# Performance work log

Measured on AMD Instinct MI355X. Metric: run time of the kernel, lower is better.

The kernel has to match this reference:

```python
import jax, jax.numpy as jnp
import numpy as np
from jax import lax

D_MODEL = 1024
D_INNER = 2048   # expand * d_model
D_STATE = 16
D_CONV = 4
DT_RANK = 64     # ceil(d_model / 16)
B_SZ, L_SEQ = 2, 2048


def setup_inputs() -> dict:
    key = jax.random.key(0)
    ks = jax.random.split(key, 12)
    s = lambda *sh: 1.0 / np.sqrt(sh[-1])
    inp = {
        "x": jax.random.normal(ks[0], (B_SZ, L_SEQ, D_MODEL), jnp.float32),
        "in_proj_w": jax.random.normal(ks[1], (2 * D_INNER, D_MODEL), jnp.float32) * s(D_MODEL),
        "conv_w": jax.random.normal(ks[2], (D_INNER, 1, D_CONV), jnp.float32) * 0.3,
        "conv_b": jax.random.normal(ks[3], (D_INNER,), jnp.float32) * 0.05,
        "x_proj_w": jax.random.normal(ks[4], (DT_RANK + 2 * D_STATE, D_INNER), jnp.float32) * s(D_INNER),
        "dt_proj_w": jax.random.normal(ks[5], (D_INNER, DT_RANK), jnp.float32) * s(DT_RANK),
        "dt_proj_b": jnp.log(jnp.exp(jax.random.uniform(ks[6], (D_INNER,), jnp.float32, 1e-3, 1e-1)) - 1.0),
        "A_log": jnp.log(jnp.broadcast_to(jnp.arange(1, D_STATE + 1, dtype=jnp.float32), (D_INNER, D_STATE))),
        "D": jnp.ones((D_INNER,), jnp.float32),
        "out_proj_w": jax.random.normal(ks[7], (D_MODEL, D_INNER), jnp.float32) * s(D_INNER),
        "ln_w": jnp.ones((D_MODEL,), jnp.float32),
        "ln_b": jnp.zeros((D_MODEL,), jnp.float32),
    }
    return inp


def _mamba(x, in_proj_w, conv_w, conv_b, x_proj_w, dt_proj_w, dt_proj_b, A_log, D, out_proj_w):
    # x: [B, L, d_model]
    xz = x @ in_proj_w.T                             # [B, L, 2*d_inner]
    u, z = jnp.split(xz, 2, axis=-1)                 # [B, L, d_inner] each
    # depthwise causal conv1d along L
    u_c = jnp.swapaxes(u, 1, 2)                      # [B, d_inner, L]
    u_c = lax.conv_general_dilated(
        u_c, conv_w, window_strides=(1,), padding=[(D_CONV - 1, 0)],
        feature_group_count=D_INNER, dimension_numbers=("NCH", "OIH", "NCH"))
    u_c = u_c + conv_b[None, :, None]
    u_c = jax.nn.silu(jnp.swapaxes(u_c, 1, 2))       # [B, L, d_inner]
    # input-dependent dt, B, C
    x_dbl = u_c @ x_proj_w.T                         # [B, L, dt_rank + 2*d_state]
    dt_lr = x_dbl[..., :DT_RANK]
    Bm = x_dbl[..., DT_RANK:DT_RANK + D_STATE]       # [B, L, d_state]
    Cm = x_dbl[..., DT_RANK + D_STATE:]              # [B, L, d_state]
    dt = jax.nn.softplus(dt_lr @ dt_proj_w.T + dt_proj_b)  # [B, L, d_inner]
    A = -jnp.exp(A_log)                              # [d_inner, d_state]

    def step(h, inputs):
        dt_t, b_t, c_t, u_t = inputs                 # [B,d_inner],[B,N],[B,N],[B,d_inner]
        dA = jnp.exp(dt_t[:, :, None] * A)           # [B, d_inner, N]
        h = h * dA + (dt_t * u_t)[:, :, None] * b_t[:, None, :]
        y_t = jnp.einsum("bdn,bn->bd", h, c_t)
        return h, y_t

    h0 = jnp.zeros((x.shape[0], D_INNER, D_STATE), x.dtype)
    xs = (jnp.swapaxes(dt, 0, 1), jnp.swapaxes(Bm, 0, 1),
          jnp.swapaxes(Cm, 0, 1), jnp.swapaxes(u_c, 0, 1))
    _, ys = lax.scan(step, h0, xs)                   # ys: [L, B, d_inner]
    y = jnp.swapaxes(ys, 0, 1) + u_c * D             # skip connection D*u
    y = y * jax.nn.silu(z)                           # gate
    return y @ out_proj_w.T                          # [B, L, d_model]


def _layernorm(x, w, b, eps=1e-5):
    mu = jnp.mean(x, axis=-1, keepdims=True)
    var = jnp.mean(jnp.square(x - mu), axis=-1, keepdims=True)
    return (x - mu) * lax.rsqrt(var + eps) * w + b


def reference(x, in_proj_w, conv_w, conv_b, x_proj_w, dt_proj_w, dt_proj_b,
              A_log, D, out_proj_w, ln_w, ln_b):
    y = _mamba(x, in_proj_w, conv_w, conv_b, x_proj_w, dt_proj_w, dt_proj_b,
               A_log, D, out_proj_w)
    return _layernorm(y + x, ln_w, ln_b)  # dropout_level=0 -> identity
```

## Files before the change

kernel.cpp:

```cpp
#include <hip/hip_runtime.h>
#include <hip/hip_bf16.h>
#include <math.h>

#define DEV static __device__ __forceinline__

typedef __hip_bfloat16 bf16;
typedef __attribute__((ext_vector_type(8))) short bf16x8;
typedef __attribute__((ext_vector_type(4))) short bf16x4;
typedef __attribute__((ext_vector_type(4))) float f32x4;

static constexpr int D_MODEL = 1024;
static constexpr int D_INNER = 2048;
static constexpr int D_STATE = 16;
static constexpr int DT_RANK = 64;
static constexpr int B_SZ   = 2;
static constexpr int L_SEQ  = 2048;
static constexpr int T_TOK  = B_SZ * L_SEQ;
static constexpr int LC     = 64;
static constexpr int NC     = L_SEQ / LC;
static constexpr int NXP    = DT_RANK + 2 * D_STATE;
static constexpr int KSPLIT = 8;

static constexpr int P_CONVW = 0;
static constexpr int P_CONVB = 8192;
static constexpr int P_DTB   = 10240;
static constexpr int P_ALOG  = 12288;
static constexpr int P_DW    = 45056;
static constexpr int P_LNW   = 47104;
static constexpr int P_LNB   = 48128;
static constexpr int P_TOT   = 49152;

DEV float bf2f(bf16 x) { return __bfloat162float(x); }
DEV bf16  f2bf(float x) { return __float2bfloat16(x); }
DEV float sigmoidf_(float x) { return 1.0f / (1.0f + __expf(-x)); }
DEV float s2f(short s) { bf16 b; __builtin_memcpy(&b, &s, 2); return bf2f(b); }
DEV short f2s(float x) { bf16 b = f2bf(x); short s; __builtin_memcpy(&s, &b, 2); return s; }

DEV bool probe_f32(const unsigned short* probe) { return probe[1] == 0; }

DEV void async_copy16(const void* g, void* l) {
  __builtin_amdgcn_global_load_lds(
      (const __attribute__((address_space(1))) void*)g,
      (__attribute__((address_space(3))) void*)l, 16, 0, 0);
}

__global__ void cvt_all(const void* s0, const void* s1, const void* s2,
                        const void* s3, const void* s4,
                        const void* s5, const void* s6, const void* s7,
                        const void* s8, const void* s9, const void* s10,
                        const void* s11,
                        bf16* d0, bf16* d1, bf16* d2, bf16* d3, bf16* d4,
                        float* params,
                        const unsigned short* __restrict__ probe)
{
  long i = (long)(blockIdx.x * 256 + threadIdx.x) * 4;
  const void* src; long off;
  bf16* dstb = nullptr; float* dstf = nullptr;
  if      (i <  4194304) { src = s0;  dstb = d0; off = i; }
  else if (i <  8388608) { src = s1;  dstb = d1; off = i - 4194304; }
  else if (i <  8585216) { src = s2;  dstb = d2; off = i - 8388608; }
  else if (i <  8716288) { src = s3;  dstb = d3; off = i - 8585216; }
  else if (i < 10813440) { src = s4;  dstb = d4; off = i - 8716288; }
  else if (i < 10821632) { src = s5;  dstf = params + P_CONVW; off = i - 10813440; }
  else if (i < 10823680) { src = s6;  dstf = params + P_CONVB; off = i - 10821632; }
  else if (i < 10825728) { src = s7;  dstf = params + P_DTB;   off = i - 10823680; }
  else if (i < 10858496) { src = s8;  dstf = params + P_ALOG;  off = i - 10825728; }
  else if (i < 10860544) { src = s9;  dstf = params + P_DW;    off = i - 10858496; }
  else if (i < 10861568) { src = s10; dstf = params + P_LNW;   off = i - 10860544; }
  else if (i < 10862592) { src = s11; dstf = params + P_LNB;   off = i - 10861568; }
  else return;
  bool isf32 = probe_f32(probe);
  float v[4];
  if (isf32) {
    float4 t = *(const float4*)((const float*)src + off);
    v[0] = t.x; v[1] = t.y; v[2] = t.z; v[3] = t.w;
  } else {
    short4 t = *(const short4*)((const bf16*)src + off);
    v[0] = s2f(t.x); v[1] = s2f(t.y); v[2] = s2f(t.z); v[3] = s2f(t.w);
  }
  if (dstb) {
    #pragma unroll
    for (int k = 0; k < 4; ++k) dstb[off + k] = f2bf(v[k]);
  } else {
    #pragma unroll
    for (int k = 0; k < 4; ++k) dstf[off + k] = v[k];
  }
}

template <int MODE>
DEV void gemm_body64(const bf16* __restrict__ A, const bf16* __restrict__ B,
                     int M, int N, int K, int ld,
                     void* __restrict__ o0, void* __restrict__ o1)
{
  __shared__ __align__(16) bf16 As[128 * 64];
  __shared__ __align__(16) bf16 Bs[128 * 64];
  if (MODE == 3) {
    A += (size_t)blockIdx.z * K;
    B += (size_t)blockIdx.z * K;
  }
  const int tid  = threadIdx.x;
  const int wave = tid >> 6;
  const int lane = tid & 63;
  const int bm = blockIdx.x * 128;
  const int bn = blockIdx.y * 128;
  const int wm = (wave >> 1) * 64;
  const int wn = (wave & 1) * 64;

  f32x4 acc[4][4];
  #pragma unroll
  for (int i = 0; i < 4; ++i)
    #pragma unroll
    for (int j = 0; j < 4; ++j)
      #pragma unroll
      for (int r = 0; r < 4; ++r) acc[i][j][r] = 0.0f;

  const int srow8 = lane >> 3;
  const int sgcol = ((lane & 7) ^ srow8) * 8;
  const int fr = lane & 15;
  const int fq = lane >> 4;

  for (int k0 = 0; k0 < K; k0 += 64) {
    __syncthreads();
    #pragma unroll
    for (int rep = 0; rep < 4; ++rep) {
      int chunk = wave * 4 + rep;
      int arow = bm + chunk * 8 + srow8;
      async_copy16((const void*)(A + (size_t)arow * ld + k0 + sgcol),
                   (void*)(As + chunk * 512));
      int brow = bn + chunk * 8 + srow8;
      if (brow > N - 1) brow = N - 1;
      async_copy16((const void*)(B + (size_t)brow * ld + k0 + sgcol),
                   (void*)(Bs + chunk * 512));
    }
    __syncthreads();

    #pragma unroll
    for (int kk = 0; kk < 2; ++kk) {
      bf16x8 af[4], bg[4];
      #pragma unroll
      for (int mi = 0; mi < 4; ++mi) {
        int row = wm + mi * 16 + fr;
        af[mi] = *(const bf16x8*)(As + row * 64 + (((kk * 4 + fq) ^ (fr & 7)) * 8));
      }
      #pragma unroll
      for (int ni = 0; ni < 4; ++ni) {
        int row = wn + ni * 16 + fr;
        bg[ni] = *(const bf16x8*)(Bs + row * 64 + (((kk * 4 + fq) ^ (fr & 7)) * 8));
      }
      #pragma unroll
      for (int mi = 0; mi < 4; ++mi)
        #pragma unroll
        for (int ni = 0; ni < 4; ++ni)
          acc[mi][ni] = __builtin_amdgcn_mfma_f32_16x16x32_bf16(af[mi], bg[ni], acc[mi][ni], 0, 0, 0);
    }
  }

  const int er = (lane >> 4) * 4;
  const int ec = lane & 15;
  #pragma unroll
  for (int mi = 0; mi < 4; ++mi) {
    #pragma unroll
    for (int ni = 0; ni < 4; ++ni) {
      #pragma unroll
      for (int r = 0; r < 4; ++r) {
        int row = bm + wm + mi * 16 + er + r;
        int col = bn + wn + ni * 16 + ec;
        float v = acc[mi][ni][r];
        if (MODE == 0) {
          if (col < D_INNER) ((bf16*)o0)[(size_t)row * D_INNER + col] = f2bf(v);
          else               ((bf16*)o1)[(size_t)row * D_INNER + (col - D_INNER)] = f2bf(v * sigmoidf_(v));
        } else {
          ((bf16*)o0)[((size_t)blockIdx.z * M + row) * D_MODEL + col] = f2bf(v);
        }
      }
    }
  }
}

template <int MODE>
DEV void gemm_body32(const bf16* __restrict__ A, const bf16* __restrict__ B,
                     int M, int N, int K, int ld,
                     void* __restrict__ o0, const void* __restrict__ e0)
{
  __shared__ __align__(16) bf16 As[128 * 32];
  __shared__ __align__(16) bf16 Bs[128 * 32];
  if (MODE == 1) {
    A += (size_t)blockIdx.z * K;
    B += (size_t)blockIdx.z * K;
  }
  const int tid  = threadIdx.x;
  const int wave = tid >> 6;
  const int lane = tid & 63;
  const int bm = blockIdx.x * 128;
  const int bn = blockIdx.y * 128;
  const int wm = (wave >> 1) * 64;
  const int wn = (wave & 1) * 64;

  f32x4 acc[4][4];
  #pragma unroll
  for (int i = 0; i < 4; ++i)
    #pragma unroll
    for (int j = 0; j < 4; ++j)
      #pragma unroll
      for (int r = 0; r < 4; ++r) acc[i][j][r] = 0.0f;

  const int ar0 = tid >> 2;
  const int ar1 = ar0 + 64;
  const int ac  = (tid & 3) * 8;
  const int fr = lane & 15;
  const int fk = (lane >> 4) * 8;

  for (int k0 = 0; k0 < K; k0 += 32) {
    bf16x8 a0 = *(const bf16x8*)(A + (size_t)(bm + ar0) * ld + k0 + ac);
    bf16x8 a1 = *(const bf16x8*)(A + (size_t)(bm + ar1) * ld + k0 + ac);
    int r0 = bn + ar0; if (r0 > N - 1) r0 = N - 1;
    int r1 = bn + ar1; if (r1 > N - 1) r1 = N - 1;
    bf16x8 b0 = *(const bf16x8*)(B + (size_t)r0 * ld + k0 + ac);
    bf16x8 b1 = *(const bf16x8*)(B + (size_t)r1 * ld + k0 + ac);
    __syncthreads();
    *(bf16x8*)(As + ar0 * 32 + ac) = a0;
    *(bf16x8*)(As + ar1 * 32 + ac) = a1;
    *(bf16x8*)(Bs + ar0 * 32 + ac) = b0;
    *(bf16x8*)(Bs + ar1 * 32 + ac) = b1;
    __syncthreads();

    bf16x8 af[4], bg[4];
    #pragma unroll
    for (int mi = 0; mi < 4; ++mi)
      af[mi] = *(const bf16x8*)(As + (wm + mi * 16 + fr) * 32 + fk);
    #pragma unroll
    for (int ni = 0; ni < 4; ++ni)
      bg[ni] = *(const bf16x8*)(Bs + (wn + ni * 16 + fr) * 32 + fk);
    #pragma unroll
    for (int mi = 0; mi < 4; ++mi)
      #pragma unroll
      for (int ni = 0; ni < 4; ++ni)
        acc[mi][ni] = __builtin_amdgcn_mfma_f32_16x16x32_bf16(af[mi], bg[ni], acc[mi][ni], 0, 0, 0);
  }

  const int er = (lane >> 4) * 4;
  const int ec = lane & 15;
  #pragma unroll
  for (int mi = 0; mi < 4; ++mi) {
    #pragma unroll
    for (int ni = 0; ni < 4; ++ni) {
      #pragma unroll
      for (int r = 0; r < 4; ++r) {
        int row = bm + wm + mi * 16 + er + r;
        int col = bn + wn + ni * 16 + ec;
        if (col >= N) continue;
        float v = acc[mi][ni][r];
        if (MODE == 1) {
          ((float*)o0)[((size_t)blockIdx.z * M + row) * N + col] = v;
        } else {
          v += ((const float*)e0)[col];
          float sp = (v > 15.0f) ? v : __logf(1.0f + __expf(v));
          ((bf16*)o0)[(size_t)row * D_INNER + col] = f2bf(sp);
        }
      }
    }
  }
}

__global__ void __launch_bounds__(256) k_inproj(const bf16* A, const bf16* B,
    void* o0, void* o1) {
  gemm_body64<0>(A, B, T_TOK, 2 * D_INNER, D_MODEL, D_MODEL, o0, o1);
}
__global__ void __launch_bounds__(256) k_outproj(const bf16* A, const bf16* B,
    void* o0) {
  gemm_body64<3>(A, B, T_TOK, D_MODEL, D_INNER / 2, D_INNER, o0, nullptr);
}
__global__ void __launch_bounds__(256) k_xproj(const bf16* A, const bf16* B,
    void* o0) {
  gemm_body32<1>(A, B, T_TOK, NXP, D_INNER / KSPLIT, D_INNER, o0, nullptr);
}
__global__ void __launch_bounds__(256) k_dtproj(const bf16* A, const bf16* B,
    void* o0, const void* e0) {
  gemm_body32<2>(A, B, T_TOK, D_INNER, DT_RANK, DT_RANK, o0, e0);
}

__global__ void xproj_post(const float* __restrict__ partials,
                           bf16* __restrict__ dtlr,
                           float* __restrict__ Bbuf,
                           float* __restrict__ Cbuf)
{
  int i = blockIdx.x * 256 + threadIdx.x;
  int col = i % NXP;
  int row = i / NXP;
  float s = 0.0f;
  #pragma unroll
  for (int kz = 0; kz < KSPLIT; ++kz)
    s += partials[((size_t)kz * T_TOK + row) * NXP + col];
  if      (col < DT_RANK)            dtlr[(size_t)row * DT_RANK + col] = f2bf(s);
  else if (col < DT_RANK + D_STATE)  Bbuf[(size_t)row * D_STATE + (col - DT_RANK)] = s;
  else                               Cbuf[(size_t)row * D_STATE + (col - DT_RANK - D_STATE)] = s;
}

__global__ void conv_silu_kernel(const bf16* __restrict__ u_pre,
                                 const float* __restrict__ cw,
                                 const float* __restrict__ cb,
                                 bf16* __restrict__ uc_bf)
{
  int idx = blockIdx.x * 256 + threadIdx.x;
  int d4 = (idx * 4) & (D_INNER - 1);
  int t  = (idx * 4) >> 11;
  int l  = t & (L_SEQ - 1);
  float4 bias = *(const float4*)(cb + d4);
  float acc[4] = {bias.x, bias.y, bias.z, bias.w};
  float4 wv[4];
  #pragma unroll
  for (int i = 0; i < 4; ++i) wv[i] = *(const float4*)(cw + (d4 + i) * 4);
  #pragma unroll
  for (int w = 0; w < 4; ++w) {
    if (l - 3 + w >= 0) {
      bf16x4 u = *(const bf16x4*)(u_pre + (size_t)(t - 3 + w) * D_INNER + d4);
      float uf[4];
      #pragma unroll
      for (int i = 0; i < 4; ++i) { short su = u[i]; uf[i] = s2f(su); }
      acc[0] += uf[0] * ((const float*)&wv[0])[w];
      acc[1] += uf[1] * ((const float*)&wv[1])[w];
      acc[2] += uf[2] * ((const float*)&wv[2])[w];
      acc[3] += uf[3] * ((const float*)&wv[3])[w];
    }
  }
  bf16x4 out;
  #pragma unroll
  for (int i = 0; i < 4; ++i) out[i] = f2s(acc[i] * sigmoidf_(acc[i]));
  *(bf16x4*)(uc_bf + (size_t)t * D_INNER + d4) = out;
}

DEV void load_Ad(const float* A_log, int d, float* Ad, bool& fast) {
  fast = true;
  #pragma unroll
  for (int n = 0; n < 16; ++n) {
    Ad[n] = -__expf(A_log[d * 16 + n]);
    fast = fast && (fabsf(Ad[n] + (float)(n + 1)) < 1e-3f * (n + 1));
  }
}
DEV void compute_decay(bool fast, float dtv, const float* Ad, float* dec) {
  if (fast) {
    float e1 = __expf(-dtv);
    float en = e1;
    #pragma unroll
    for (int n = 0; n < 16; ++n) { dec[n] = en; en *= e1; }
  } else {
    #pragma unroll
    for (int n = 0; n < 16; ++n) dec[n] = __expf(Ad[n] * dtv);
  }
}

__global__ __launch_bounds__(256) void scan_pass1(
    const bf16* __restrict__ dt, const bf16* __restrict__ uc_bf,
    const float* __restrict__ Bbuf, const float* __restrict__ A_log,
    float* __restrict__ hend, float* __restrict__ sumdt)
{
  __shared__ float Bs4[LC * D_STATE];
  __shared__ bf16 dts[16 * 256];
  __shared__ bf16 uts[16 * 256];
  int bid = blockIdx.x;
  int tid = threadIdx.x;
  int dt8 = bid & 7;
  int c = (bid >> 3) & (NC - 1);
  int b = bid >> 8;
  int d0 = dt8 * 256;
  int d  = d0 + tid;
  int t0g = b * L_SEQ + c * LC;

  ((f32x4*)Bs4)[tid] = ((const f32x4*)(Bbuf + (size_t)t0g * D_STATE))[tid];

  float Ad[16], h[16];
  bool fast;
  load_Ad(A_log, d, Ad, fast);
  #pragma unroll
  for (int n = 0; n < 16; ++n) h[n] = 0.0f;
  float sdt = 0.0f;

  for (int sub = 0; sub < 4; ++sub) {
    __syncthreads();
    #pragma unroll
    for (int rep = 0; rep < 2; ++rep) {
      int idx = rep * 256 + tid;
      int row = idx >> 5;
      int col = (idx & 31) * 8;
      size_t src = (size_t)(t0g + sub * 16 + row) * D_INNER + d0 + col;
      *(bf16x8*)(dts + row * 256 + col) = *(const bf16x8*)(dt + src);
      *(bf16x8*)(uts + row * 256 + col) = *(const bf16x8*)(uc_bf + src);
    }
    __syncthreads();
    for (int t = 0; t < 16; ++t) {
      float dtv = bf2f(dts[t * 256 + tid]);
      float uv  = bf2f(uts[t * 256 + tid]);
      float su  = dtv * uv;
      sdt += dtv;
      float dec[16];
      compute_decay(fast, dtv, Ad, dec);
      const float* Bp = Bs4 + (sub * 16 + t) * 16;
      #pragma unroll
      for (int n = 0; n < 16; ++n)
        h[n] = h[n] * dec[n] + su * Bp[n];
    }
  }
  size_t base = ((size_t)(b * NC + c) * D_INNER + d) * 16;
  #pragma unroll
  for (int q = 0; q < 4; ++q)
    *(f32x4*)(hend + base + q * 4) = *(f32x4*)(h + q * 4);
  sumdt[(size_t)(b * NC + c) * D_INNER + d] = sdt;
}

__global__ __launch_bounds__(256) void scan_pass2(
    float* __restrict__ hend, const float* __restrict__ sumdt,
    const float* __restrict__ A_log)
{
  __shared__ float Ms[4][64];
  __shared__ float Es[4][64];
  int bid = blockIdx.x;
  int tid = threadIdx.x;
  int cg   = tid >> 6;
  int lane = tid & 63;
  int dloc = lane >> 4;
  int n    = lane & 15;
  int b     = bid >> 9;
  int d     = (bid & 511) * 4 + dloc;

  float a = -__expf(A_log[d * 16 + n]);

  float Ml[8], El[8];
  float M = 1.0f, E = 0.0f;
  #pragma unroll
  for (int j = 0; j < 8; ++j) {
    int c = cg * 8 + j;
    size_t sbase = (size_t)(b * NC + c) * D_INNER + d;
    float m = __expf(a * sumdt[sbase]);
    float e = hend[sbase * 16 + n];
    Ml[j] = M; El[j] = E;
    M = m * M;
    E = m * E + e;
  }
  Ms[cg][lane] = M;
  Es[cg][lane] = E;
  __syncthreads();
  float Ep = 0.0f;
  for (int g = 0; g < cg; ++g) {
    float Mg = Ms[g][lane], Eg = Es[g][lane];
    Ep = Mg * Ep + Eg;
  }
  #pragma unroll
  for (int j = 0; j < 8; ++j) {
    int c = cg * 8 + j;
    size_t sbase = (size_t)(b * NC + c) * D_INNER + d;
    hend[sbase * 16 + n] = Ml[j] * Ep + El[j];
  }
}

__global__ __launch_bounds__(256) void scan_pass3(
    const bf16* __restrict__ dt, const bf16* __restrict__ uc_bf,
    const float* __restrict__ Bbuf, const float* __restrict__ Cbuf,
    const bf16* __restrict__ z_silu, const float* __restrict__ hstart,
    const float* __restrict__ A_log, const float* __restrict__ Dw,
    bf16* __restrict__ y_bf)
{
  __shared__ float Bs4[LC * D_STATE];
  __shared__ float Cs4[LC * D_STATE];
  __shared__ bf16 dts[16 * 256];
  __shared__ bf16 uts[16 * 256];
  __shared__ bf16 zts[16 * 256];
  int bid = blockIdx.x;
  int tid = threadIdx.x;
  int dt8 = bid & 7;
  int c = (bid >> 3) & (NC - 1);
  int b = bid >> 8;
  int d0 = dt8 * 256;
  int d  = d0 + tid;
  int t0g = b * L_SEQ + c * LC;

  ((f32x4*)Bs4)[tid] = ((const f32x4*)(Bbuf + (size_t)t0g * D_STATE))[tid];
  ((f32x4*)Cs4)[tid] = ((const f32x4*)(Cbuf + (size_t)t0g * D_STATE))[tid];

  float Ad[16], h[16];
  bool fast;
  load_Ad(A_log, d, Ad, fast);
  size_t base = ((size_t)(b * NC + c) * D_INNER + d) * 16;
  #pragma unroll
  for (int q = 0; q < 4; ++q)
    *(f32x4*)(h + q * 4) = *(const f32x4*)(hstart + base + q * 4);
  float Dv = Dw[d];

  for (int sub = 0; sub < 4; ++sub) {
    __syncthreads();
    #pragma unroll
    for (int rep = 0; rep < 2; ++rep) {
      int idx = rep * 256 + tid;
      int row = idx >> 5;
      int col = (idx & 31) * 8;
      size_t src = (size_t)(t0g + sub * 16 + row) * D_INNER + d0 + col;
      *(bf16x8*)(dts + row * 256 + col) = *(const bf16x8*)(dt + src);
      *(bf16x8*)(uts + row * 256 + col) = *(const bf16x8*)(uc_bf + src);
      *(bf16x8*)(zts + row * 256 + col) = *(const bf16x8*)(z_silu + src);
    }
    __syncthreads();
    for (int t = 0; t < 16; ++t) {
      float dtv = bf2f(dts[t * 256 + tid]);
      float uv  = bf2f(uts[t * 256 + tid]);
      float zv  = bf2f(zts[t * 256 + tid]);
      float su  = dtv * uv;
      float dec[16];
      compute_decay(fast, dtv, Ad, dec);
      const float* Bp = Bs4 + (sub * 16 + t) * 16;
      const float* Cp = Cs4 + (sub * 16 + t) * 16;
      float y = 0.0f;
      #pragma unroll
      for (int n = 0; n < 16; ++n) {
        h[n] = h[n] * dec[n] + su * Bp[n];
        y += h[n] * Cp[n];
      }
      y = (y + uv * Dv) * zv;
      y_bf[(size_t)(t0g + sub * 16 + t) * D_INNER + d] = f2bf(y);
    }
  }
}

__global__ void ln_kernel(const bf16* __restrict__ parts,
                          const bf16* __restrict__ x_bf,
                          const float* __restrict__ w,
                          const float* __restrict__ bia,
                          void* __restrict__ out,
                          const unsigned short* __restrict__ probe)
{
  int t = blockIdx.x;
  int tid = threadIdx.x;
  const bf16* p0 = parts + (size_t)t * D_MODEL;
  const bf16* p1 = parts + ((size_t)T_TOK + t) * D_MODEL;
  const bf16* xr = x_bf + (size_t)t * D_MODEL;
  float v[4];
  float s = 0.0f, q = 0.0f;
  #pragma unroll
  for (int k = 0; k < 4; ++k) {
    int col = tid + k * 256;
    v[k] = bf2f(p0[col]) + bf2f(p1[col]) + bf2f(xr[col]);
    s += v[k]; q += v[k] * v[k];
  }
  #pragma unroll
  for (int off = 32; off >= 1; off >>= 1) {
    s += __shfl_down(s, off);
    q += __shfl_down(q, off);
  }
  __shared__ float red[8];
  __shared__ float mv[2];
  int wave = tid >> 6, lane = tid & 63;
  if (lane == 0) { red[wave] = s; red[4 + wave] = q; }
  __syncthreads();
  if (tid == 0) {
    float S = red[0] + red[1] + red[2] + red[3];
    float Q = red[4] + red[5] + red[6] + red[7];
    float mu = S * (1.0f / D_MODEL);
    float var = Q * (1.0f / D_MODEL) - mu * mu;
    mv[0] = mu; mv[1] = rsqrtf(var + 1e-5f);
  }
  __syncthreads();
  float mu = mv[0], rs = mv[1];
  bool isf32 = probe_f32(probe);
  #pragma unroll
  for (int k = 0; k < 4; ++k) {
    int col = tid + k * 256;
    float r = (v[k] - mu) * rs * w[col] + bia[col];
    if (isf32) ((float*)out)[(size_t)t * D_MODEL + col] = r;
    else       ((bf16*) out)[(size_t)t * D_MODEL + col] = f2bf(r);
  }
}

extern "C" void kernel_launch(void* const* d_in, const int* in_sizes, int n_in,
                              void* d_out, int out_size, void* d_ws, size_t ws_size,
                              hipStream_t stream)
{
  const void* x        = d_in[0];
  const void* in_w     = d_in[1];
  const void* conv_w   = d_in[2];
  const void* conv_b   = d_in[3];
  const void* xproj_w  = d_in[4];
  const void* dtproj_w = d_in[5];
  const void* dtproj_b = d_in[6];
  const void* A_log    = d_in[7];
  const void* Dw       = d_in[8];
  const void* out_w    = d_in[9];
  const void* ln_w     = d_in[10];
  const void* ln_b     = d_in[11];
  const unsigned short* probe = (const unsigned short*)A_log;

  char* p = (char*)d_ws;
  auto alloc = [&](size_t bytes) { char* r = p; p += (bytes + 255) & ~255ull; return r; };
  bf16*  x_bf   = (bf16*) alloc((size_t)T_TOK * D_MODEL * 2);
  bf16*  inw_bf = (bf16*) alloc((size_t)2 * D_INNER * D_MODEL * 2);
  bf16*  xpw_bf = (bf16*) alloc((size_t)NXP * D_INNER * 2);
  bf16*  dtw_bf = (bf16*) alloc((size_t)D_INNER * DT_RANK * 2);
  bf16*  outw_bf= (bf16*) alloc((size_t)D_MODEL * D_INNER * 2);
  float* params = (float*)alloc((size_t)P_TOT * 4);
  bf16*  u_pre  = (bf16*) alloc((size_t)T_TOK * D_INNER * 2);
  bf16*  z_silu = (bf16*) alloc((size_t)T_TOK * D_INNER * 2);
  bf16*  uc_bf  = (bf16*) alloc((size_t)T_TOK * D_INNER * 2);
  bf16*  dtlr   = (bf16*) alloc((size_t)T_TOK * DT_RANK * 2);
  float* Bbuf   = (float*)alloc((size_t)T_TOK * D_STATE * 4);
  float* Cbuf   = (float*)alloc((size_t)T_TOK * D_STATE * 4);
  bf16*  dtb    = (bf16*) alloc((size_t)T_TOK * D_INNER * 2);
  float* hend   = (float*)alloc((size_t)B_SZ * NC * D_INNER * 16 * 4);
  float* sumdt  = (float*)alloc((size_t)B_SZ * NC * D_INNER * 4);
  bf16*  y_bf   = u_pre;
  float* xparts = (float*)dtb;
  bf16*  oparts = z_silu;

  dim3 blk(256);
  cvt_all<<<10608, blk, 0, stream>>>(x, in_w, xproj_w, dtproj_w, out_w,
                                     conv_w, conv_b, dtproj_b, A_log, Dw, ln_w, ln_b,
                                     x_bf, inw_bf, xpw_bf, dtw_bf, outw_bf, params, probe);

  k_inproj<<<dim3(T_TOK / 128, (2 * D_INNER) / 128), blk, 0, stream>>>(x_bf, inw_bf, u_pre, z_silu);
  conv_silu_kernel<<<(T_TOK * D_INNER) / 1024, blk, 0, stream>>>(u_pre, params + P_CONVW, params + P_CONVB, uc_bf);
  k_xproj<<<dim3(T_TOK / 128, 1, KSPLIT), blk, 0, stream>>>(uc_bf, xpw_bf, xparts);
  xproj_post<<<(T_TOK * NXP) / 256, blk, 0, stream>>>(xparts, dtlr, Bbuf, Cbuf);
  k_dtproj<<<dim3(T_TOK / 128, D_INNER / 128), blk, 0, stream>>>(dtlr, dtw_bf, dtb, params + P_DTB);
  scan_pass1<<<B_SZ * NC * (D_INNER / 256), blk, 0, stream>>>(dtb, uc_bf, Bbuf, params + P_ALOG, hend, sumdt);
  scan_pass2<<<(B_SZ * D_INNER) / 2, blk, 0, stream>>>(hend, sumdt, params + P_ALOG);
  scan_pass3<<<B_SZ * NC * (D_INNER / 256), blk, 0, stream>>>(
      dtb, uc_bf, Bbuf, Cbuf, z_silu, hend, params + P_ALOG, params + P_DW, y_bf);
  k_outproj<<<dim3(T_TOK / 128, D_MODEL / 128, 2), blk, 0, stream>>>(y_bf, outw_bf, oparts);
  ln_kernel<<<T_TOK, blk, 0, stream>>>(oparts, x_bf, params + P_LNW, params + P_LNB, d_out, probe);
}
```

Baseline: 307.1 us.

## Pipeline in/out projection GEMMs with 4-slot async LDS ring and 8 waves

```diff
diff --git a/kernel.cpp b/kernel.cpp
--- a/kernel.cpp
+++ b/kernel.cpp
@@ -42,6 +42,13 @@
   __builtin_amdgcn_global_load_lds(
       (const __attribute__((address_space(1))) void*)g,
       (__attribute__((address_space(3))) void*)l, 16, 0, 0);
+}
+
+template <int N>
+DEV void vm_wait() {
+  if constexpr (N == 6)      asm volatile("s_waitcnt vmcnt(6)" ::: "memory");
+  else if constexpr (N == 3) asm volatile("s_waitcnt vmcnt(3)" ::: "memory");
+  else                       asm volatile("s_waitcnt vmcnt(0)" ::: "memory");
 }
 
 __global__ void cvt_all(const void* s0, const void* s1, const void* s2,
@@ -87,13 +94,37 @@
   }
 }
 
+static constexpr int SLOT_BYTES = 256 * 32 * 2 + 128 * 32 * 2;
+static constexpr int B_OFF      = 256 * 32 * 2;
+
+DEV void stage_slot(const bf16* __restrict__ A, const bf16* __restrict__ B,
+                    int ld, int bm, int bn, int k0,
+                    char* slot, int wave, int lane)
+{
+  const int tid = wave * 64 + lane;
+  #pragma unroll
+  for (int j = 0; j < 2; ++j) {
+    int p   = j * 8192 + tid * 16;
+    int row = p >> 6;
+    int ckl = ((p >> 4) & 3) ^ (row & 3);
+    async_copy16(A + (size_t)(bm + row) * ld + k0 + ckl * 8,
+                 slot + j * 8192 + wave * 1024);
+  }
+  {
+    int p   = tid * 16;
+    int row = p >> 6;
+    int ckl = ((p >> 4) & 3) ^ (row & 3);
+    async_copy16(B + (size_t)(bn + row) * ld + k0 + ckl * 8,
+                 slot + B_OFF + wave * 1024);
+  }
+}
+
 template <int MODE>
-DEV void gemm_body64(const bf16* __restrict__ A, const bf16* __restrict__ B,
+DEV void gemm8p_body(const bf16* __restrict__ A, const bf16* __restrict__ B,
                      int M, int N, int K, int ld,
                      void* __restrict__ o0, void* __restrict__ o1)
 {
-  __shared__ __align__(16) bf16 As[128 * 64];
-  __shared__ __align__(16) bf16 Bs[128 * 64];
+  __shared__ __align__(16) char ring[4 * SLOT_BYTES];
   if (MODE == 3) {
     A += (size_t)blockIdx.z * K;
     B += (size_t)blockIdx.z * K;
@@ -101,10 +132,16 @@
   const int tid  = threadIdx.x;
   const int wave = tid >> 6;
   const int lane = tid & 63;
-  const int bm = blockIdx.x * 128;
+  const int bm = blockIdx.x * 256;
   const int bn = blockIdx.y * 128;
-  const int wm = (wave >> 1) * 64;
-  const int wn = (wave & 1) * 64;
+  const int wm = wave >> 1;
+  const int wn = wave & 1;
+  const int fr = lane & 15;
+  const int fg = lane >> 4;
+  const int sck = ((fg ^ (fr & 3)) << 4);
+  const int abase = (wm * 64 + fr) * 64 + sck;
+  const int bbase = B_OFF + (wn * 64 + fr) * 64 + sck;
+  const int NT = K / 32;
 
   f32x4 acc[4][4];
   #pragma unroll
@@ -114,45 +151,41 @@
       #pragma unroll
       for (int r = 0; r < 4; ++r) acc[i][j][r] = 0.0f;
 
-  const int srow8 = lane >> 3;
-  const int sgcol = ((lane & 7) ^ srow8) * 8;
-  const int fr = lane & 15;
-  const int fq = lane >> 4;
-
-  for (int k0 = 0; k0 < K; k0 += 64) {
-    __syncthreads();
-    #pragma unroll
-    for (int rep = 0; rep < 4; ++rep) {
-      int chunk = wave * 4 + rep;
-      int arow = bm + chunk * 8 + srow8;
-      async_copy16((const void*)(A + (size_t)arow * ld + k0 + sgcol),
-                   (void*)(As + chunk * 512));
-      int brow = bn + chunk * 8 + srow8;
-      if (brow > N - 1) brow = N - 1;
-      async_copy16((const void*)(B + (size_t)brow * ld + k0 + sgcol),
-                   (void*)(Bs + chunk * 512));
-    }
-    __syncthreads();
-
-    #pragma unroll
-    for (int kk = 0; kk < 2; ++kk) {
-      bf16x8 af[4], bg[4];
-      #pragma unroll
-      for (int mi = 0; mi < 4; ++mi) {
-        int row = wm + mi * 16 + fr;
-        af[mi] = *(const bf16x8*)(As + row * 64 + (((kk * 4 + fq) ^ (fr & 7)) * 8));
-      }
-      #pragma unroll
-      for (int ni = 0; ni < 4; ++ni) {
-        int row = wn + ni * 16 + fr;
-        bg[ni] = *(const bf16x8*)(Bs + row * 64 + (((kk * 4 + fq) ^ (fr & 7)) * 8));
-      }
-      #pragma unroll
-      for (int mi = 0; mi < 4; ++mi)
-        #pragma unroll
-        for (int ni = 0; ni < 4; ++ni)
-          acc[mi][ni] = __builtin_amdgcn_mfma_f32_16x16x32_bf16(af[mi], bg[ni], acc[mi][ni], 0, 0, 0);
-    }
+  #pragma unroll
+  for (int u = 0; u < 3; ++u)
+    stage_slot(A, B, ld, bm, bn, u * 32, ring + u * SLOT_BYTES, wave, lane);
+
+  for (int t = 0; t < NT; ++t) {
+    if (t < NT - 2)       vm_wait<6>();
+    else if (t == NT - 2) vm_wait<3>();
+    else                  vm_wait<0>();
+    __builtin_amdgcn_sched_barrier(0);
+    __builtin_amdgcn_s_barrier();
+    __builtin_amdgcn_sched_barrier(0);
+
+    const char* sb = ring + (t & 3) * SLOT_BYTES;
+    bf16x8 af[4], bg[4];
+    #pragma unroll
+    for (int mi = 0; mi < 4; ++mi)
+      af[mi] = *(const bf16x8*)(sb + abase + mi * 1024);
+    #pragma unroll
+    for (int ni = 0; ni < 4; ++ni)
+      bg[ni] = *(const bf16x8*)(sb + bbase + ni * 1024);
+    __builtin_amdgcn_sched_barrier(0);
+
+    if (t + 3 < NT)
+      stage_slot(A, B, ld, bm, bn, (t + 3) * 32,
+                 ring + ((t + 3) & 3) * SLOT_BYTES, wave, lane);
+    __builtin_amdgcn_sched_barrier(0);
+
+    __builtin_amdgcn_s_setprio(1);
+    #pragma unroll
+    for (int mi = 0; mi < 4; ++mi)
+      #pragma unroll
+      for (int ni = 0; ni < 4; ++ni)
+        acc[mi][ni] = __builtin_amdgcn_mfma_f32_16x16x32_bf16(af[mi], bg[ni], acc[mi][ni], 0, 0, 0);
+    __builtin_amdgcn_s_setprio(0);
+    __builtin_amdgcn_sched_barrier(0);
   }
 
   const int er = (lane >> 4) * 4;
@@ -163,8 +196,8 @@
     for (int ni = 0; ni < 4; ++ni) {
       #pragma unroll
       for (int r = 0; r < 4; ++r) {
-        int row = bm + wm + mi * 16 + er + r;
-        int col = bn + wn + ni * 16 + ec;
+        int row = bm + wm * 64 + mi * 16 + er + r;
+        int col = bn + wn * 64 + ni * 16 + ec;
         float v = acc[mi][ni][r];
         if (MODE == 0) {
           if (col < D_INNER) ((bf16*)o0)[(size_t)row * D_INNER + col] = f2bf(v);
@@ -262,13 +295,13 @@
   }
 }
 
-__global__ void __launch_bounds__(256) k_inproj(const bf16* A, const bf16* B,
+__global__ void __launch_bounds__(512) k_inproj(const bf16* A, const bf16* B,
     void* o0, void* o1) {
-  gemm_body64<0>(A, B, T_TOK, 2 * D_INNER, D_MODEL, D_MODEL, o0, o1);
-}
-__global__ void __launch_bounds__(256) k_outproj(const bf16* A, const bf16* B,
+  gemm8p_body<0>(A, B, T_TOK, 2 * D_INNER, D_MODEL, D_MODEL, o0, o1);
+}
+__global__ void __launch_bounds__(512) k_outproj(const bf16* A, const bf16* B,
     void* o0) {
-  gemm_body64<3>(A, B, T_TOK, D_MODEL, D_INNER / 2, D_INNER, o0, nullptr);
+  gemm8p_body<3>(A, B, T_TOK, D_MODEL, D_INNER / 2, D_INNER, o0, nullptr);
 }
 __global__ void __launch_bounds__(256) k_xproj(const bf16* A, const bf16* B,
     void* o0) {
@@ -608,11 +641,12 @@
   bf16*  oparts = z_silu;
 
   dim3 blk(256);
+  dim3 blk512(512);
   cvt_all<<<10608, blk, 0, stream>>>(x, in_w, xproj_w, dtproj_w, out_w,
                                      conv_w, conv_b, dtproj_b, A_log, Dw, ln_w, ln_b,
                                      x_bf, inw_bf, xpw_bf, dtw_bf, outw_bf, params, probe);
 
-  k_inproj<<<dim3(T_TOK / 128, (2 * D_INNER) / 128), blk, 0, stream>>>(x_bf, inw_bf, u_pre, z_silu);
+  k_inproj<<<dim3(T_TOK / 256, (2 * D_INNER) / 128), blk512, 0, stream>>>(x_bf, inw_bf, u_pre, z_silu);
   conv_silu_kernel<<<(T_TOK * D_INNER) / 1024, blk, 0, stream>>>(u_pre, params + P_CONVW, params + P_CONVB, uc_bf);
   k_xproj<<<dim3(T_TOK / 128, 1, KSPLIT), blk, 0, stream>>>(uc_bf, xpw_bf, xparts);
   xproj_post<<<(T_TOK * NXP) / 256, blk, 0, stream>>>(xparts, dtlr, Bbuf, Cbuf);
@@ -621,6 +655,6 @@
   scan_pass2<<<(B_SZ * D_INNER) / 2, blk, 0, stream>>>(hend, sumdt, params + P_ALOG);
   scan_pass3<<<B_SZ * NC * (D_INNER / 256), blk, 0, stream>>>(
       dtb, uc_bf, Bbuf, Cbuf, z_silu, hend, params + P_ALOG, params + P_DW, y_bf);
-  k_outproj<<<dim3(T_TOK / 128, D_MODEL / 128, 2), blk, 0, stream>>>(y_bf, outw_bf, oparts);
+  k_outproj<<<dim3(T_TOK / 256, D_MODEL / 128, 2), blk512, 0, stream>>>(y_bf, outw_bf, oparts);
   ln_kernel<<<T_TOK, blk, 0, stream>>>(oparts, x_bf, params + P_LNW, params + P_LNB, d_out, probe);
 }
```

After: 311.3 us. No clear change (+1.4%).

## Pipeline in/out-proj GEMMs with triple-buffered LDS ring and 256x128 tiles

Applied to the files above, without the earlier changes.

```diff
diff --git a/kernel.cpp b/kernel.cpp
--- a/kernel.cpp
+++ b/kernel.cpp
@@ -42,6 +42,12 @@
   __builtin_amdgcn_global_load_lds(
       (const __attribute__((address_space(1))) void*)g,
       (__attribute__((address_space(3))) void*)l, 16, 0, 0);
+}
+
+template <int N>
+DEV void vm_wait() {
+  if constexpr (N == 6) asm volatile("s_waitcnt vmcnt(6)" ::: "memory");
+  else                  asm volatile("s_waitcnt vmcnt(0)" ::: "memory");
 }
 
 __global__ void cvt_all(const void* s0, const void* s1, const void* s2,
@@ -87,13 +93,39 @@
   }
 }
 
+static constexpr int SLOT = 48 * 1024;
+static constexpr int BOFF = 32 * 1024;
+
+DEV void stage_A(const bf16* __restrict__ A, int ld, int bm, int k0,
+                 char* slot, int tid) {
+  #pragma unroll
+  for (int j = 0; j < 4; ++j) {
+    int p   = j * 8192 + tid * 16;
+    int row = p >> 7;
+    int ck  = ((p >> 4) & 7) ^ (row & 7);
+    async_copy16(A + (size_t)(bm + row) * ld + k0 + ck * 8,
+                 slot + j * 8192 + (tid >> 6) * 1024);
+  }
+}
+
+DEV void stage_B(const bf16* __restrict__ B, int ld, int bn, int k0,
+                 char* slot, int tid) {
+  #pragma unroll
+  for (int j = 0; j < 2; ++j) {
+    int p   = j * 8192 + tid * 16;
+    int row = p >> 7;
+    int ck  = ((p >> 4) & 7) ^ (row & 7);
+    async_copy16(B + (size_t)(bn + row) * ld + k0 + ck * 8,
+                 slot + BOFF + j * 8192 + (tid >> 6) * 1024);
+  }
+}
+
 template <int MODE>
-DEV void gemm_body64(const bf16* __restrict__ A, const bf16* __restrict__ B,
-                     int M, int N, int K, int ld,
-                     void* __restrict__ o0, void* __restrict__ o1)
-{
-  __shared__ __align__(16) bf16 As[128 * 64];
-  __shared__ __align__(16) bf16 Bs[128 * 64];
+DEV void gemm_pipe(const bf16* __restrict__ A, const bf16* __restrict__ B,
+                   int M, int K, int ld,
+                   void* __restrict__ o0, void* __restrict__ o1)
+{
+  __shared__ __align__(16) char ring[3 * SLOT];
   if (MODE == 3) {
     A += (size_t)blockIdx.z * K;
     B += (size_t)blockIdx.z * K;
@@ -101,58 +133,96 @@
   const int tid  = threadIdx.x;
   const int wave = tid >> 6;
   const int lane = tid & 63;
-  const int bm = blockIdx.x * 128;
+  const int bm = blockIdx.x * 256;
   const int bn = blockIdx.y * 128;
   const int wm = (wave >> 1) * 64;
   const int wn = (wave & 1) * 64;
-
-  f32x4 acc[4][4];
-  #pragma unroll
-  for (int i = 0; i < 4; ++i)
-    #pragma unroll
-    for (int j = 0; j < 4; ++j)
-      #pragma unroll
-      for (int r = 0; r < 4; ++r) acc[i][j][r] = 0.0f;
-
-  const int srow8 = lane >> 3;
-  const int sgcol = ((lane & 7) ^ srow8) * 8;
   const int fr = lane & 15;
   const int fq = lane >> 4;
-
-  for (int k0 = 0; k0 < K; k0 += 64) {
-    __syncthreads();
-    #pragma unroll
-    for (int rep = 0; rep < 4; ++rep) {
-      int chunk = wave * 4 + rep;
-      int arow = bm + chunk * 8 + srow8;
-      async_copy16((const void*)(A + (size_t)arow * ld + k0 + sgcol),
-                   (void*)(As + chunk * 512));
-      int brow = bn + chunk * 8 + srow8;
-      if (brow > N - 1) brow = N - 1;
-      async_copy16((const void*)(B + (size_t)brow * ld + k0 + sgcol),
-                   (void*)(Bs + chunk * 512));
-    }
-    __syncthreads();
-
-    #pragma unroll
-    for (int kk = 0; kk < 2; ++kk) {
-      bf16x8 af[4], bg[4];
-      #pragma unroll
-      for (int mi = 0; mi < 4; ++mi) {
+  const int NT = K / 64;
+
+  f32x4 acc[4][4];
+  #pragma unroll
+  for (int i = 0; i < 4; ++i)
+    #pragma unroll
+    for (int j = 0; j < 4; ++j)
+      #pragma unroll
+      for (int r = 0; r < 4; ++r) acc[i][j][r] = 0.0f;
+
+  stage_A(A, ld, bm, 0,  ring,        tid);
+  stage_B(B, ld, bn, 0,  ring,        tid);
+  stage_A(A, ld, bm, 64, ring + SLOT, tid);
+  stage_B(B, ld, bn, 64, ring + SLOT, tid);
+
+  int scur = 0;
+  #pragma unroll 1
+  for (int tk = 0; tk < NT; ++tk) {
+    if (tk < NT - 1) vm_wait<6>();
+    else             vm_wait<0>();
+    __builtin_amdgcn_sched_barrier(0);
+    __builtin_amdgcn_s_barrier();
+    __builtin_amdgcn_sched_barrier(0);
+
+    const char* sa = ring + scur * SLOT;
+    int snxt = scur + 2; if (snxt >= 3) snxt -= 3;
+    char* sn = ring + snxt * SLOT;
+
+    bf16x8 af[4][2], bg[2][2];
+    #pragma unroll
+    for (int mi = 0; mi < 4; ++mi)
+      #pragma unroll
+      for (int kk = 0; kk < 2; ++kk) {
         int row = wm + mi * 16 + fr;
-        af[mi] = *(const bf16x8*)(As + row * 64 + (((kk * 4 + fq) ^ (fr & 7)) * 8));
+        af[mi][kk] = *(const bf16x8*)(sa + row * 128 + (((kk * 4 + fq) ^ (fr & 7)) * 16));
       }
-      #pragma unroll
-      for (int ni = 0; ni < 4; ++ni) {
+    #pragma unroll
+    for (int ni = 0; ni < 2; ++ni)
+      #pragma unroll
+      for (int kk = 0; kk < 2; ++kk) {
         int row = wn + ni * 16 + fr;
-        bg[ni] = *(const bf16x8*)(Bs + row * 64 + (((kk * 4 + fq) ^ (fr & 7)) * 8));
+        bg[ni][kk] = *(const bf16x8*)(sa + BOFF + row * 128 + (((kk * 4 + fq) ^ (fr & 7)) * 16));
       }
+    __builtin_amdgcn_sched_barrier(0);
+    if (tk + 2 < NT) stage_A(A, ld, bm, (tk + 2) * 64, sn, tid);
+    __builtin_amdgcn_sched_barrier(0);
+    asm volatile("s_waitcnt lgkmcnt(0)" ::: "memory");
+    __builtin_amdgcn_sched_barrier(0);
+    __builtin_amdgcn_s_setprio(1);
+    #pragma unroll
+    for (int kk = 0; kk < 2; ++kk)
       #pragma unroll
       for (int mi = 0; mi < 4; ++mi)
         #pragma unroll
-        for (int ni = 0; ni < 4; ++ni)
-          acc[mi][ni] = __builtin_amdgcn_mfma_f32_16x16x32_bf16(af[mi], bg[ni], acc[mi][ni], 0, 0, 0);
-    }
+        for (int ni = 0; ni < 2; ++ni)
+          acc[mi][ni] = __builtin_amdgcn_mfma_f32_16x16x32_bf16(af[mi][kk], bg[ni][kk], acc[mi][ni], 0, 0, 0);
+    __builtin_amdgcn_s_setprio(0);
+    __builtin_amdgcn_sched_barrier(0);
+
+    bf16x8 bh[2][2];
+    #pragma unroll
+    for (int ni = 0; ni < 2; ++ni)
+      #pragma unroll
+      for (int kk = 0; kk < 2; ++kk) {
+        int row = wn + (ni + 2) * 16 + fr;
+        bh[ni][kk] = *(const bf16x8*)(sa + BOFF + row * 128 + (((kk * 4 + fq) ^ (fr & 7)) * 16));
+      }
+    __builtin_amdgcn_sched_barrier(0);
+    if (tk + 2 < NT) stage_B(B, ld, bn, (tk + 2) * 64, sn, tid);
+    __builtin_amdgcn_sched_barrier(0);
+    asm volatile("s_waitcnt lgkmcnt(0)" ::: "memory");
+    __builtin_amdgcn_sched_barrier(0);
+    __builtin_amdgcn_s_setprio(1);
+    #pragma unroll
+    for (int kk = 0; kk < 2; ++kk)
+      #pragma unroll
+      for (int mi = 0; mi < 4; ++mi)
+        #pragma unroll
+        for (int ni = 0; ni < 2; ++ni)
+          acc[mi][ni + 2] = __builtin_amdgcn_mfma_f32_16x16x32_bf16(af[mi][kk], bh[ni][kk], acc[mi][ni + 2], 0, 0, 0);
+    __builtin_amdgcn_s_setprio(0);
+    __builtin_amdgcn_sched_barrier(0);
+
+    scur = (scur + 1 == 3) ? 0 : scur + 1;
   }
 
   const int er = (lane >> 4) * 4;
@@ -262,13 +332,13 @@
   }
 }
 
-__global__ void __launch_bounds__(256) k_inproj(const bf16* A, const bf16* B,
+__global__ void __launch_bounds__(512) k_inproj(const bf16* A, const bf16* B,
     void* o0, void* o1) {
-  gemm_body64<0>(A, B, T_TOK, 2 * D_INNER, D_MODEL, D_MODEL, o0, o1);
-}
-__global__ void __launch_bounds__(256) k_outproj(const bf16* A, const bf16* B,
+  gemm_pipe<0>(A, B, T_TOK, D_MODEL, D_MODEL, o0, o1);
+}
+__global__ void __launch_bounds__(512) k_outproj(const bf16* A, const bf16* B,
     void* o0) {
-  gemm_body64<3>(A, B, T_TOK, D_MODEL, D_INNER / 2, D_INNER, o0, nullptr);
+  gemm_pipe<3>(A, B, T_TOK, D_INNER / 2, D_INNER, o0, nullptr);
 }
 __global__ void __launch_bounds__(256) k_xproj(const bf16* A, const bf16* B,
     void* o0) {
@@ -608,11 +678,12 @@
   bf16*  oparts = z_silu;
 
   dim3 blk(256);
+  dim3 blk512(512);
   cvt_all<<<10608, blk, 0, stream>>>(x, in_w, xproj_w, dtproj_w, out_w,
                                      conv_w, conv_b, dtproj_b, A_log, Dw, ln_w, ln_b,
                                      x_bf, inw_bf, xpw_bf, dtw_bf, outw_bf, params, probe);
 
-  k_inproj<<<dim3(T_TOK / 128, (2 * D_INNER) / 128), blk, 0, stream>>>(x_bf, inw_bf, u_pre, z_silu);
+  k_inproj<<<dim3(T_TOK / 256, (2 * D_INNER) / 128), blk512, 0, stream>>>(x_bf, inw_bf, u_pre, z_silu);
   conv_silu_kernel<<<(T_TOK * D_INNER) / 1024, blk, 0, stream>>>(u_pre, params + P_CONVW, params + P_CONVB, uc_bf);
   k_xproj<<<dim3(T_TOK / 128, 1, KSPLIT), blk, 0, stream>>>(uc_bf, xpw_bf, xparts);
   xproj_post<<<(T_TOK * NXP) / 256, blk, 0, stream>>>(xparts, dtlr, Bbuf, Cbuf);
@@ -621,6 +692,6 @@
   scan_pass2<<<(B_SZ * D_INNER) / 2, blk, 0, stream>>>(hend, sumdt, params + P_ALOG);
   scan_pass3<<<B_SZ * NC * (D_INNER / 256), blk, 0, stream>>>(
       dtb, uc_bf, Bbuf, Cbuf, z_silu, hend, params + P_ALOG, params + P_DW, y_bf);
-  k_outproj<<<dim3(T_TOK / 128, D_MODEL / 128, 2), blk, 0, stream>>>(y_bf, outw_bf, oparts);
+  k_outproj<<<dim3(T_TOK / 256, D_MODEL / 128, 2), blk512, 0, stream>>>(y_bf, outw_bf, oparts);
   ln_kernel<<<T_TOK, blk, 0, stream>>>(oparts, x_bf, params + P_LNW, params + P_LNB, d_out, probe);
 }
```

After: 307.7 us. About the same (+0.2%).

## Replace in/out projection GEMMs with double-buffered 256x256 async-LDS pipeline

Applied to the files above, without the earlier changes.

```diff
diff --git a/kernel.cpp b/kernel.cpp
--- a/kernel.cpp
+++ b/kernel.cpp
@@ -42,6 +42,13 @@
   __builtin_amdgcn_global_load_lds(
       (const __attribute__((address_space(1))) void*)g,
       (__attribute__((address_space(3))) void*)l, 16, 0, 0);
+}
+
+template <int N>
+DEV void vm_wait() {
+  if constexpr (N == 8)      asm volatile("s_waitcnt vmcnt(8)" ::: "memory");
+  else if constexpr (N == 6) asm volatile("s_waitcnt vmcnt(6)" ::: "memory");
+  else                       asm volatile("s_waitcnt vmcnt(0)" ::: "memory");
 }
 
 __global__ void cvt_all(const void* s0, const void* s1, const void* s2,
@@ -87,13 +94,50 @@
   }
 }
 
+DEV void stage256(const bf16* __restrict__ src, int ld, int base_row, int k0,
+                  char* dst_base, int tid) {
+  #pragma unroll
+  for (int j = 0; j < 4; ++j) {
+    int p   = j * 8192 + tid * 16;
+    int row = p >> 7;
+    int ck  = ((p >> 4) & 7) ^ (row & 7);
+    async_copy16(src + (size_t)(base_row + row) * ld + k0 + ck * 8,
+                 dst_base + j * 8192 + (tid >> 6) * 1024);
+  }
+}
+
+#define PHASE(MH, KK, LOADB)                                                  \
+  {                                                                           \
+    _Pragma("unroll")                                                         \
+    for (int mi = 0; mi < 4; ++mi)                                            \
+      af[mi] = *(const bf16x8*)(sa + ((size_t)(wmr + (MH)*64 + mi*16 + fr))*128 \
+                                + (((((KK)*4+fq)) ^ frs) * 16));              \
+    if (LOADB) {                                                              \
+      _Pragma("unroll")                                                       \
+      for (int ni = 0; ni < 4; ++ni)                                          \
+        bg[ni] = *(const bf16x8*)(sa + 32768 + ((size_t)(wnr + ni*16 + fr))*128 \
+                                  + (((((KK)*4+fq)) ^ frs) * 16));            \
+    }                                                                         \
+    __builtin_amdgcn_sched_barrier(0);                                        \
+    asm volatile("s_waitcnt lgkmcnt(0)" ::: "memory");                        \
+    __builtin_amdgcn_sched_barrier(0);                                        \
+    __builtin_amdgcn_s_setprio(1);                                            \
+    _Pragma("unroll")                                                         \
+    for (int mi = 0; mi < 4; ++mi)                                            \
+      _Pragma("unroll")                                                       \
+      for (int ni = 0; ni < 4; ++ni)                                          \
+        acc[(MH)*4+mi][ni] = __builtin_amdgcn_mfma_f32_16x16x32_bf16(         \
+            af[mi], bg[ni], acc[(MH)*4+mi][ni], 0, 0, 0);                     \
+    __builtin_amdgcn_s_setprio(0);                                            \
+    __builtin_amdgcn_sched_barrier(0);                                        \
+  }
+
 template <int MODE>
-DEV void gemm_body64(const bf16* __restrict__ A, const bf16* __restrict__ B,
-                     int M, int N, int K, int ld,
-                     void* __restrict__ o0, void* __restrict__ o1)
-{
-  __shared__ __align__(16) bf16 As[128 * 64];
-  __shared__ __align__(16) bf16 Bs[128 * 64];
+DEV void gemm_pipe256(const bf16* __restrict__ A, const bf16* __restrict__ B,
+                      int M, int K, int ld,
+                      void* __restrict__ o0, void* __restrict__ o1)
+{
+  __shared__ __align__(16) char ring[2 * 65536];
   if (MODE == 3) {
     A += (size_t)blockIdx.z * K;
     B += (size_t)blockIdx.z * K;
@@ -101,76 +145,69 @@
   const int tid  = threadIdx.x;
   const int wave = tid >> 6;
   const int lane = tid & 63;
-  const int bm = blockIdx.x * 128;
-  const int bn = blockIdx.y * 128;
-  const int wm = (wave >> 1) * 64;
-  const int wn = (wave & 1) * 64;
-
-  f32x4 acc[4][4];
-  #pragma unroll
-  for (int i = 0; i < 4; ++i)
-    #pragma unroll
-    for (int j = 0; j < 4; ++j)
-      #pragma unroll
-      for (int r = 0; r < 4; ++r) acc[i][j][r] = 0.0f;
-
-  const int srow8 = lane >> 3;
-  const int sgcol = ((lane & 7) ^ srow8) * 8;
+  const int bm = blockIdx.x * 256;
+  const int bn = blockIdx.y * 256;
+  const int wmr = (wave >> 2) * 128;
+  const int wnr = (wave & 3) * 64;
   const int fr = lane & 15;
   const int fq = lane >> 4;
-
-  for (int k0 = 0; k0 < K; k0 += 64) {
-    __syncthreads();
-    #pragma unroll
-    for (int rep = 0; rep < 4; ++rep) {
-      int chunk = wave * 4 + rep;
-      int arow = bm + chunk * 8 + srow8;
-      async_copy16((const void*)(A + (size_t)arow * ld + k0 + sgcol),
-                   (void*)(As + chunk * 512));
-      int brow = bn + chunk * 8 + srow8;
-      if (brow > N - 1) brow = N - 1;
-      async_copy16((const void*)(B + (size_t)brow * ld + k0 + sgcol),
-                   (void*)(Bs + chunk * 512));
-    }
-    __syncthreads();
-
-    #pragma unroll
-    for (int kk = 0; kk < 2; ++kk) {
-      bf16x8 af[4], bg[4];
-      #pragma unroll
-      for (int mi = 0; mi < 4; ++mi) {
-        int row = wm + mi * 16 + fr;
-        af[mi] = *(const bf16x8*)(As + row * 64 + (((kk * 4 + fq) ^ (fr & 7)) * 8));
-      }
-      #pragma unroll
-      for (int ni = 0; ni < 4; ++ni) {
-        int row = wn + ni * 16 + fr;
-        bg[ni] = *(const bf16x8*)(Bs + row * 64 + (((kk * 4 + fq) ^ (fr & 7)) * 8));
-      }
-      #pragma unroll
-      for (int mi = 0; mi < 4; ++mi)
-        #pragma unroll
-        for (int ni = 0; ni < 4; ++ni)
-          acc[mi][ni] = __builtin_amdgcn_mfma_f32_16x16x32_bf16(af[mi], bg[ni], acc[mi][ni], 0, 0, 0);
+  const int frs = lane & 7;
+  const int NT = K / 64;
+
+  f32x4 acc[8][4];
+  #pragma unroll
+  for (int i = 0; i < 8; ++i)
+    #pragma unroll
+    for (int j = 0; j < 4; ++j)
+      #pragma unroll
+      for (int r = 0; r < 4; ++r) acc[i][j][r] = 0.0f;
+
+  stage256(A, ld, bm, 0,  ring,                 tid);
+  stage256(B, ld, bn, 0,  ring + 32768,         tid);
+  stage256(A, ld, bm, 64, ring + 65536,         tid);
+  stage256(B, ld, bn, 64, ring + 65536 + 32768, tid);
+
+  #pragma unroll 1
+  for (int tk = 0; tk < NT; ++tk) {
+    if (tk < NT - 1) vm_wait<8>();
+    else             vm_wait<0>();
+    __builtin_amdgcn_sched_barrier(0);
+    __builtin_amdgcn_s_barrier();
+    __builtin_amdgcn_sched_barrier(0);
+
+    const char* sa = ring + (size_t)(tk & 1) * 65536;
+    bf16x8 af[4], bg[4];
+    PHASE(0, 0, true)
+    PHASE(1, 0, false)
+    PHASE(0, 1, true)
+    PHASE(1, 1, false)
+
+    __builtin_amdgcn_s_barrier();
+    if (tk + 2 < NT) {
+      char* sn = ring + (size_t)(tk & 1) * 65536;
+      stage256(A, ld, bm, (tk + 2) * 64, sn,         tid);
+      stage256(B, ld, bn, (tk + 2) * 64, sn + 32768, tid);
     }
   }
 
   const int er = (lane >> 4) * 4;
   const int ec = lane & 15;
   #pragma unroll
-  for (int mi = 0; mi < 4; ++mi) {
+  for (int ai = 0; ai < 8; ++ai) {
     #pragma unroll
     for (int ni = 0; ni < 4; ++ni) {
       #pragma unroll
       for (int r = 0; r < 4; ++r) {
-        int row = bm + wm + mi * 16 + er + r;
-        int col = bn + wn + ni * 16 + ec;
-        float v = acc[mi][ni][r];
+        int row = bm + wmr + ai * 16 + er + r;
+        int col = bn + wnr + ni * 16 + ec;
+        float v = acc[ai][ni][r];
         if (MODE == 0) {
           if (col < D_INNER) ((bf16*)o0)[(size_t)row * D_INNER + col] = f2bf(v);
           else               ((bf16*)o1)[(size_t)row * D_INNER + (col - D_INNER)] = f2bf(v * sigmoidf_(v));
         } else {
-          ((bf16*)o0)[((size_t)blockIdx.z * M + row) * D_MODEL + col] = f2bf(v);
+          int zz = blockIdx.z;
+          bf16* dst = (zz < 2) ? (bf16*)o0 : (bf16*)o1;
+          dst[(((size_t)(zz & 1)) * M + row) * D_MODEL + col] = f2bf(v);
         }
       }
     }
@@ -262,13 +299,13 @@
   }
 }
 
-__global__ void __launch_bounds__(256) k_inproj(const bf16* A, const bf16* B,
+__global__ void __launch_bounds__(512, 2) k_inproj(const bf16* A, const bf16* B,
     void* o0, void* o1) {
-  gemm_body64<0>(A, B, T_TOK, 2 * D_INNER, D_MODEL, D_MODEL, o0, o1);
-}
-__global__ void __launch_bounds__(256) k_outproj(const bf16* A, const bf16* B,
-    void* o0) {
-  gemm_body64<3>(A, B, T_TOK, D_MODEL, D_INNER / 2, D_INNER, o0, nullptr);
+  gemm_pipe256<0>(A, B, T_TOK, D_MODEL, D_MODEL, o0, o1);
+}
+__global__ void __launch_bounds__(512, 2) k_outproj(const bf16* A, const bf16* B,
+    void* o0, void* o1) {
+  gemm_pipe256<3>(A, B, T_TOK, D_INNER / 4, D_INNER, o0, o1);
 }
 __global__ void __launch_bounds__(256) k_xproj(const bf16* A, const bf16* B,
     void* o0) {
@@ -519,7 +556,8 @@
   }
 }
 
-__global__ void ln_kernel(const bf16* __restrict__ parts,
+__global__ void ln_kernel(const bf16* __restrict__ partsA,
+                          const bf16* __restrict__ partsB,
                           const bf16* __restrict__ x_bf,
                           const float* __restrict__ w,
                           const float* __restrict__ bia,
@@ -528,15 +566,17 @@
 {
   int t = blockIdx.x;
   int tid = threadIdx.x;
-  const bf16* p0 = parts + (size_t)t * D_MODEL;
-  const bf16* p1 = parts + ((size_t)T_TOK + t) * D_MODEL;
+  const bf16* p0 = partsA + (size_t)t * D_MODEL;
+  const bf16* p1 = partsA + ((size_t)T_TOK + t) * D_MODEL;
+  const bf16* p2 = partsB + (size_t)t * D_MODEL;
+  const bf16* p3 = partsB + ((size_t)T_TOK + t) * D_MODEL;
   const bf16* xr = x_bf + (size_t)t * D_MODEL;
   float v[4];
   float s = 0.0f, q = 0.0f;
   #pragma unroll
   for (int k = 0; k < 4; ++k) {
     int col = tid + k * 256;
-    v[k] = bf2f(p0[col]) + bf2f(p1[col]) + bf2f(xr[col]);
+    v[k] = bf2f(p0[col]) + bf2f(p1[col]) + bf2f(p2[col]) + bf2f(p3[col]) + bf2f(xr[col]);
     s += v[k]; q += v[k] * v[k];
   }
   #pragma unroll
@@ -605,14 +645,16 @@
   float* sumdt  = (float*)alloc((size_t)B_SZ * NC * D_INNER * 4);
   bf16*  y_bf   = u_pre;
   float* xparts = (float*)dtb;
-  bf16*  oparts = z_silu;
+  bf16*  opartsA = z_silu;
+  bf16*  opartsB = dtb;
 
   dim3 blk(256);
+  dim3 blk512(512);
   cvt_all<<<10608, blk, 0, stream>>>(x, in_w, xproj_w, dtproj_w, out_w,
                                      conv_w, conv_b, dtproj_b, A_log, Dw, ln_w, ln_b,
                                      x_bf, inw_bf, xpw_bf, dtw_bf, outw_bf, params, probe);
 
-  k_inproj<<<dim3(T_TOK / 128, (2 * D_INNER) / 128), blk, 0, stream>>>(x_bf, inw_bf, u_pre, z_silu);
+  k_inproj<<<dim3(T_TOK / 256, (2 * D_INNER) / 256), blk512, 0, stream>>>(x_bf, inw_bf, u_pre, z_silu);
   conv_silu_kernel<<<(T_TOK * D_INNER) / 1024, blk, 0, stream>>>(u_pre, params + P_CONVW, params + P_CONVB, uc_bf);
   k_xproj<<<dim3(T_TOK / 128, 1, KSPLIT), blk, 0, stream>>>(uc_bf, xpw_bf, xparts);
   xproj_post<<<(T_TOK * NXP) / 256, blk, 0, stream>>>(xparts, dtlr, Bbuf, Cbuf);
@@ -621,6 +663,6 @@
   scan_pass2<<<(B_SZ * D_INNER) / 2, blk, 0, stream>>>(hend, sumdt, params + P_ALOG);
   scan_pass3<<<B_SZ * NC * (D_INNER / 256), blk, 0, stream>>>(
       dtb, uc_bf, Bbuf, Cbuf, z_silu, hend, params + P_ALOG, params + P_DW, y_bf);
-  k_outproj<<<dim3(T_TOK / 128, D_MODEL / 128, 2), blk, 0, stream>>>(y_bf, outw_bf, oparts);
-  ln_kernel<<<T_TOK, blk, 0, stream>>>(oparts, x_bf, params + P_LNW, params + P_LNB, d_out, probe);
-}
+  k_outproj<<<dim3(T_TOK / 256, D_MODEL / 256, 4), blk512, 0, stream>>>(y_bf, outw_bf, opartsA, opartsB);
+  ln_kernel<<<T_TOK, blk, 0, stream>>>(opartsA, opartsB, x_bf, params + P_LNW, params + P_LNB, d_out, probe);
+}
```

Measured after the change: 305.9 us. No clear change (-0.4%).
